# Optimization experiments

Measured on AMD Instinct MI355X. Metric: run time of the kernel, lower is better.

The kernel has to match this reference:

```python
import jax, jax.numpy as jnp
import numpy as np

D_MODEL = 1024
D_HIDDEN = 4096
NUM_EXPERTS = 8
K_ACTIVE = 2


def setup_inputs() -> dict:
    key = jax.random.key(0)
    ks = jax.random.split(key, 8)
    x = jax.random.normal(ks[0], (1, 2048, D_MODEL), dtype=jnp.float32)
    gate_w = jax.random.normal(ks[1], (D_MODEL, NUM_EXPERTS), dtype=jnp.float32) * 0.02
    gate_b = jnp.zeros((NUM_EXPERTS,), dtype=jnp.float32)
    w1 = jax.random.normal(ks[2], (NUM_EXPERTS, D_MODEL, D_HIDDEN), dtype=jnp.float32) * 0.02
    b1 = jnp.zeros((NUM_EXPERTS, D_HIDDEN), dtype=jnp.float32)
    w2 = jax.random.normal(ks[3], (NUM_EXPERTS, D_HIDDEN, D_MODEL), dtype=jnp.float32) * 0.02
    b2 = jnp.zeros((NUM_EXPERTS, D_MODEL), dtype=jnp.float32)
    return {"x": x, "gate_w": gate_w, "gate_b": gate_b,
            "w1": w1, "b1": b1, "w2": w2, "b2": b2}


def reference(x, gate_w, gate_b, w1, b1, w2, b2):
    B, S, D = x.shape
    xf = x.reshape(-1, D)                                    # [T, D]
    logits = xf @ gate_w + gate_b                            # [T, E]
    top_w, top_idx = jax.lax.top_k(logits, K_ACTIVE)         # [T, K]
    top_w = jax.nn.softmax(top_w, axis=-1)                   # softmax over selected experts
    # combine-weight per expert: sum over k slots of one-hot(idx) * weight -> [T, E]
    gates = jnp.sum(jax.nn.one_hot(top_idx, NUM_EXPERTS, dtype=xf.dtype) * top_w[..., None], axis=1)
    # expert FFN applied per expert (dropout is identity in eval): gelu is exact (erf), matching torch nn.GELU default
    h = jax.nn.gelu(jnp.einsum('td,edh->teh', xf, w1) + b1[None], approximate=False)  # [T, E, H]
    y = jnp.einsum('teh,ehd->ted', h, w2) + b2[None]         # [T, E, D]
    out = jnp.einsum('ted,te->td', y, gates)                 # weighted combine of selected experts
    return out.reshape(B, S, D)
```

## Files before the change

### kernel.cpp

```cpp
#include <hip/hip_runtime.h>
#include <stdint.h>

typedef unsigned short u16;
typedef __attribute__((ext_vector_type(8))) short s16x8;
typedef __attribute__((ext_vector_type(8))) u16  u16x8;
typedef __attribute__((ext_vector_type(4))) u16  u16x4;
typedef __attribute__((ext_vector_type(4))) float f32x4;

#define T_TOKENS 2048
#define DM 1024
#define DH 4096
#define NE 8
#define BK 64
#define PAD2 256
#define MAXS2 (T_TOKENS*2 + NE*PAD2)
#define RB1 (MAXS2/256)
#define RB2 (MAXS2/128)
#define BM 128
#define BN 128
#define MAXSLOTS (T_TOKENS*2 + NE*BM)
#define ROWBLK (MAXSLOTS/BM)

__device__ __forceinline__ u16 f2bf(float f) {
    union { float ff; uint32_t u; } v; v.ff = f;
    uint32_t r = v.u + 0x7fffu + ((v.u >> 16) & 1u);
    return (u16)(r >> 16);
}

#define GLOAD_LDS16(gsrc, ldst) \
    __builtin_amdgcn_global_load_lds((const __attribute__((address_space(1))) uint32_t*)(gsrc), \
                                     (__attribute__((address_space(3))) uint32_t*)(ldst), 16, 0, 0)

#define WAIT_VM8() asm volatile("s_waitcnt vmcnt(8)" ::: "memory")
#define WAIT_VM0() asm volatile("s_waitcnt vmcnt(0)" ::: "memory")

__global__ void k_convert(const float* __restrict__ x, u16* __restrict__ xbf,
                          int* __restrict__ ctrl) {
    int i = blockIdx.x * blockDim.x + threadIdx.x;
    const f32x4* xv = (const f32x4*)x;
    f32x4 a = xv[2*i], b = xv[2*i+1];
    u16x8 o;
    o[0]=f2bf(a[0]); o[1]=f2bf(a[1]); o[2]=f2bf(a[2]); o[3]=f2bf(a[3]);
    o[4]=f2bf(b[0]); o[5]=f2bf(b[1]); o[6]=f2bf(b[2]); o[7]=f2bf(b[3]);
    ((u16x8*)xbf)[i] = o;
    if (blockIdx.x == 0 && threadIdx.x < 32) ctrl[threadIdx.x] = 0;
}

__global__ void __launch_bounds__(256) k_transpose(const float* __restrict__ src,
                                                   u16* __restrict__ dst,
                                                   int K, int N, int nw0, int NW) {
    __shared__ float tile[64][65];
    const int e = blockIdx.z;
    const int n0 = nw0 + blockIdx.x * 64, k0 = blockIdx.y * 64;
    const float* s = src + (size_t)e * K * N;
    u16* d = dst + (size_t)e * K * NW;
    const int tx = threadIdx.x & 15, ty = threadIdx.x >> 4;
    #pragma unroll
    for (int j = 0; j < 4; ++j) {
        int r = ty * 4 + j;
        f32x4 v = *(const f32x4*)(s + (size_t)(k0 + r) * N + n0 + tx * 4);
        tile[r][tx*4+0] = v[0]; tile[r][tx*4+1] = v[1];
        tile[r][tx*4+2] = v[2]; tile[r][tx*4+3] = v[3];
    }
    __syncthreads();
    #pragma unroll
    for (int j = 0; j < 4; ++j) {
        int n = ty * 4 + j;
        u16x4 w;
        #pragma unroll
        for (int c = 0; c < 4; ++c) w[c] = f2bf(tile[tx*4+c][n]);
        *(u16x4*)(d + (size_t)(n0 - nw0 + n) * K + k0 + tx * 4) = w;
    }
}

__global__ void __launch_bounds__(64) k_gate(const float* __restrict__ x,
                                             const float* __restrict__ gw,
                                             const float* __restrict__ gb,
                                             int* __restrict__ cnt,
                                             int* __restrict__ tt_idx,
                                             float* __restrict__ tt_w) {
    const int t = blockIdx.x;
    const int lane = threadIdx.x;
    float acc[NE] = {0.f,0.f,0.f,0.f,0.f,0.f,0.f,0.f};
    const float* xr = x + (size_t)t * DM;
    #pragma unroll
    for (int c = 0; c < DM/64; ++c) {
        float xv = xr[lane + 64*c];
        const float* g = gw + (size_t)(lane + 64*c) * NE;
        #pragma unroll
        for (int e = 0; e < NE; ++e) acc[e] += xv * g[e];
    }
    #pragma unroll
    for (int e = 0; e < NE; ++e) {
        #pragma unroll
        for (int off = 32; off >= 1; off >>= 1)
            acc[e] += __shfl_xor(acc[e], off, 64);
    }
    if (lane == 0) {
        float l[NE];
        #pragma unroll
        for (int e = 0; e < NE; ++e) l[e] = acc[e] + gb[e];
        int i0 = 0;
        #pragma unroll
        for (int e = 1; e < NE; ++e) if (l[e] > l[i0]) i0 = e;
        int i1 = (i0 == 0) ? 1 : 0;
        #pragma unroll
        for (int e = 0; e < NE; ++e) if (e != i0 && l[e] > l[i1]) i1 = e;
        float m  = l[i0];
        float w0 = expf(l[i0] - m), w1 = expf(l[i1] - m);
        float s = w0 + w1; w0 /= s; w1 /= s;
        tt_idx[t*2] = i0; tt_idx[t*2+1] = i1;
        tt_w[t*2] = w0;  tt_w[t*2+1] = w1;
        atomicAdd(&cnt[i0], 1); atomicAdd(&cnt[i1], 1);
    }
}

__global__ void k_offsets(const int* __restrict__ cnt, int* __restrict__ fill,
                          int* __restrict__ off, int pad) {
    if (threadIdx.x == 0 && blockIdx.x == 0) {
        int a = 0;
        for (int e = 0; e < NE; ++e) {
            off[e] = a;
            a += (cnt[e] + pad - 1) / pad * pad;
            fill[e] = 0;
        }
        off[NE] = a;
    }
}

__global__ void k_scatter(const int* __restrict__ tt_idx, const float* __restrict__ tt_w,
                          const int* __restrict__ off, int* __restrict__ fill,
                          int* __restrict__ slot_token, float* __restrict__ slot_gate) {
    int t = blockIdx.x * blockDim.x + threadIdx.x;
    if (t >= T_TOKENS) return;
    #pragma unroll
    for (int k = 0; k < 2; ++k) {
        int e = tt_idx[t*2+k];
        int pos = off[e] + atomicAdd(&fill[e], 1);
        slot_token[pos] = t;
        slot_gate[pos]  = tt_w[t*2+k];
    }
}

__device__ __forceinline__ void mma64(const u16* As, const u16* Bs, int lane,
                                      int wr, int wc, f32x4 acc[4][4]) {
    #pragma unroll
    for (int ko = 0; ko < 2; ++ko) {
        s16x8 af[4], bfr[4];
        #pragma unroll
        for (int m = 0; m < 4; ++m) {
            int row = wr*64 + m*16 + (lane & 15);
            int sl = (ko*4 + (lane >> 4)) ^ (row & 7);
            af[m] = *(const s16x8*)&As[row*BK + sl*8];
        }
        #pragma unroll
        for (int n = 0; n < 4; ++n) {
            int col = wc*64 + n*16 + (lane & 15);
            int sl = (ko*4 + (lane >> 4)) ^ (col & 7);
            bfr[n] = *(const s16x8*)&Bs[col*BK + sl*8];
        }
        #pragma unroll
        for (int m = 0; m < 4; ++m)
            #pragma unroll
            for (int n = 0; n < 4; ++n)
                acc[m][n] = __builtin_amdgcn_mfma_f32_16x16x32_bf16(af[m], bfr[n], acc[m][n], 0, 0, 0);
    }
}

__global__ void __launch_bounds__(512, 4) k_ffn1_b16(
    const u16* __restrict__ xbf, const u16* __restrict__ wt,
    const float* __restrict__ b1, const int* __restrict__ slot_token,
    const int* __restrict__ off, u16* __restrict__ h, int cb0, int NW)
{
    __shared__ u16 As[256*BK];
    __shared__ u16 Bs[128*BK];
    const int rb = blockIdx.y, cbl = blockIdx.x;
    const int total = off[NE];
    const int r0 = rb * 256;
    if (r0 >= total) return;
    int e = 0;
    while (e < NE-1 && off[e+1] <= r0) e++;
    const u16* Bsrc = wt + (size_t)e * DM * NW;
    const float* be = b1 + (size_t)e * DH;
    const int colbase = (cb0 + cbl) * 128;

    const int tid = threadIdx.x;
    const int lane = tid & 63, wid = tid >> 6;
    const int wr = wid >> 1, wc = wid & 1;

    const u16* gA[4]; const u16* gB[2];
    #pragma unroll
    for (int i = 0; i < 4; ++i) {
        int row = wid*32 + i*8 + (lane >> 3);
        int g = (lane & 7) ^ (row & 7);
        int tok = slot_token[r0 + row];
        gA[i] = xbf + (size_t)tok * DM + g*8;
    }
    #pragma unroll
    for (int i = 0; i < 2; ++i) {
        int n = wid*16 + i*8 + (lane >> 3);
        int g = (lane & 7) ^ (n & 7);
        gB[i] = Bsrc + (size_t)(cbl*128 + n) * DM + g*8;
    }

    f32x4 acc[4][4];
    #pragma unroll
    for (int m = 0; m < 4; ++m)
        #pragma unroll
        for (int n = 0; n < 4; ++n) acc[m][n] = (f32x4){0.f,0.f,0.f,0.f};

    const int NT = DM / BK;
    #pragma unroll 1
    for (int kt = 0; kt < NT; ++kt) {
        #pragma unroll
        for (int i = 0; i < 4; ++i)
            GLOAD_LDS16(gA[i] + kt*BK, &As[(wid*32 + i*8)*BK]);
        #pragma unroll
        for (int i = 0; i < 2; ++i)
            GLOAD_LDS16(gB[i] + kt*BK, &Bs[(wid*16 + i*8)*BK]);
        __syncthreads();
        mma64(As, Bs, lane, wr, wc, acc);
        __syncthreads();
    }

    #pragma unroll
    for (int n = 0; n < 4; ++n) {
        int col = colbase + wc*64 + n*16 + (lane & 15);
        float bb = be[col];
        #pragma unroll
        for (int m = 0; m < 4; ++m) {
            int rbase = r0 + wr*64 + m*16 + (lane >> 4)*4;
            #pragma unroll
            for (int i = 0; i < 4; ++i) {
                float v = acc[m][n][i] + bb;
                float gv = 0.5f * v * (1.0f + erff(v * 0.70710678118654752f));
                h[(size_t)(rbase + i)*DH + col] = f2bf(gv);
            }
        }
    }
}

__global__ void __launch_bounds__(256) k_ffn2_b16(
    const u16* __restrict__ h, const u16* __restrict__ w2t,
    const float* __restrict__ b2, const int* __restrict__ slot_token,
    const float* __restrict__ slot_gate, const int* __restrict__ off,
    float* __restrict__ out)
{
    __shared__ u16 As[2][BM*BK];
    __shared__ u16 Bs[2][BN*BK];
    const int rb = blockIdx.y, cb = blockIdx.x;
    const int total = off[NE];
    const int r0 = rb * BM;
    if (r0 >= total) return;
    int e = 0;
    while (e < NE-1 && off[e+1] <= r0) e++;
    const u16* Bsrc = w2t + (size_t)e * DH * DM;
    const float* be = b2 + (size_t)e * DM;

    const int tid = threadIdx.x;
    const int lane = tid & 63, wid = tid >> 6;
    const int wr = wid >> 1, wc = wid & 1;

    const u16* gA[4]; const u16* gB[4];
    #pragma unroll
    for (int i = 0; i < 4; ++i) {
        int row = wid*32 + i*8 + (lane >> 3);
        int g = (lane & 7) ^ (row & 7);
        gA[i] = h + (size_t)(r0 + row) * DH + g*8;
        gB[i] = Bsrc + (size_t)(cb*BN + row) * DH + g*8;
    }

    f32x4 acc[4][4];
    #pragma unroll
    for (int m = 0; m < 4; ++m)
        #pragma unroll
        for (int n = 0; n < 4; ++n) acc[m][n] = (f32x4){0.f,0.f,0.f,0.f};

    #define STG2(buf, kt) do {                                                \
        _Pragma("unroll")                                                     \
        for (int i = 0; i < 4; ++i) {                                         \
            GLOAD_LDS16(gA[i] + (kt)*BK, &As[buf][(wid*32 + i*8)*BK]);        \
            GLOAD_LDS16(gB[i] + (kt)*BK, &Bs[buf][(wid*32 + i*8)*BK]);        \
        }                                                                     \
    } while (0)

    const int NT = DH / BK;
    STG2(0, 0);
    STG2(1, 1);
    #pragma unroll 1
    for (int kt = 0; kt < NT; ++kt) {
        if (kt + 1 < NT) WAIT_VM8(); else WAIT_VM0();
        __builtin_amdgcn_s_barrier();
        __builtin_amdgcn_s_setprio(1);
        mma64(As[kt & 1], Bs[kt & 1], lane, wr, wc, acc);
        __builtin_amdgcn_s_setprio(0);
        __builtin_amdgcn_s_barrier();
        if (kt + 2 < NT) STG2(kt & 1, kt + 2);
    }
    #undef STG2

    float bb[4];
    #pragma unroll
    for (int n = 0; n < 4; ++n) bb[n] = be[cb*BN + wc*64 + n*16 + (lane & 15)];
    #pragma unroll
    for (int m = 0; m < 4; ++m) {
        #pragma unroll
        for (int i = 0; i < 4; ++i) {
            int s = r0 + wr*64 + m*16 + (lane >> 4)*4 + i;
            int tok = slot_token[s];
            float g = slot_gate[s];
            if (g != 0.0f) {
                float* orow = out + (size_t)tok * DM + cb*BN + wc*64;
                #pragma unroll
                for (int n = 0; n < 4; ++n)
                    atomicAdd(orow + n*16 + (lane & 15), g * (acc[m][n][i] + bb[n]));
            }
        }
    }
}


__global__ void __launch_bounds__(256) k_ffn1_f32(
    const u16* __restrict__ xbf, const float* __restrict__ w1,
    const float* __restrict__ b1, const int* __restrict__ slot_token,
    const int* __restrict__ off, u16* __restrict__ h)
{
    __shared__ u16 As[BM*BK];
    __shared__ u16 Bs[BN*BK];
    const int rb = blockIdx.y, cb = blockIdx.x;
    const int total = off[NE];
    const int r0 = rb * BM;
    if (r0 >= total) return;
    int e = 0;
    while (e < NE-1 && off[e+1] <= r0) e++;
    const float* Bsrc = w1 + (size_t)e * DM * DH;
    const float* be   = b1 + (size_t)e * DH;

    const int tid = threadIdx.x;
    const int lane = tid & 63, wid = tid >> 6;
    const int wr = wid >> 1, wc = wid & 1;

    const u16* gA[4];
    #pragma unroll
    for (int i = 0; i < 4; ++i) {
        int row = wid*32 + i*8 + (lane >> 3);
        int g = (lane & 7) ^ (row & 7);
        int tok = slot_token[r0 + row];
        gA[i] = xbf + (size_t)tok * DM + g*8;
    }
    const int tc = tid & 31, tr = tid >> 5;
    const float* gB = Bsrc + (size_t)(tr*8) * DH + cb*BN + tc*4;

    f32x4 acc[4][4];
    #pragma unroll
    for (int m = 0; m < 4; ++m)
        #pragma unroll
        for (int n = 0; n < 4; ++n) acc[m][n] = (f32x4){0.f,0.f,0.f,0.f};

    for (int kt = 0; kt < DM/BK; ++kt) {
        #pragma unroll
        for (int i = 0; i < 4; ++i)
            GLOAD_LDS16(gA[i] + kt*BK, &As[(wid*32 + i*8)*BK]);
        f32x4 bv[8];
        #pragma unroll
        for (int j = 0; j < 8; ++j)
            bv[j] = *(const f32x4*)(gB + (size_t)(kt*BK + j) * DH);
        #pragma unroll
        for (int c = 0; c < 4; ++c) {
            int n = tc*4 + c;
            int sl = tr ^ (n & 7);
            s16x8 pk;
            #pragma unroll
            for (int j = 0; j < 8; ++j) pk[j] = (short)f2bf(bv[j][c]);
            *(s16x8*)&Bs[n*BK + sl*8] = pk;
        }
        __syncthreads();
        mma64(As, Bs, lane, wr, wc, acc);
        __syncthreads();
    }
    #pragma unroll
    for (int n = 0; n < 4; ++n) {
        int col = cb*BN + wc*64 + n*16 + (lane & 15);
        float bb = be[col];
        #pragma unroll
        for (int m = 0; m < 4; ++m) {
            int rbase = r0 + wr*64 + m*16 + (lane >> 4)*4;
            #pragma unroll
            for (int i = 0; i < 4; ++i) {
                float v = acc[m][n][i] + bb;
                float gv = 0.5f * v * (1.0f + erff(v * 0.70710678118654752f));
                h[(size_t)(rbase + i)*DH + col] = f2bf(gv);
            }
        }
    }
}

__global__ void __launch_bounds__(256) k_ffn2_f32(
    const u16* __restrict__ h, const float* __restrict__ w2,
    const float* __restrict__ b2, const int* __restrict__ slot_token,
    const float* __restrict__ slot_gate, const int* __restrict__ off,
    float* __restrict__ out)
{
    __shared__ u16 As[BM*BK];
    __shared__ u16 Bs[BN*BK];
    const int rb = blockIdx.y, cb = blockIdx.x;
    const int total = off[NE];
    const int r0 = rb * BM;
    if (r0 >= total) return;
    int e = 0;
    while (e < NE-1 && off[e+1] <= r0) e++;
    const float* Bsrc = w2 + (size_t)e * DH * DM;
    const float* be   = b2 + (size_t)e * DM;

    const int tid = threadIdx.x;
    const int lane = tid & 63, wid = tid >> 6;
    const int wr = wid >> 1, wc = wid & 1;

    const u16* gA[4];
    #pragma unroll
    for (int i = 0; i < 4; ++i) {
        int row = wid*32 + i*8 + (lane >> 3);
        int g = (lane & 7) ^ (row & 7);
        gA[i] = h + (size_t)(r0 + row) * DH + g*8;
    }
    const int tc = tid & 31, tr = tid >> 5;
    const float* gB = Bsrc + (size_t)(tr*8) * DM + cb*BN + tc*4;

    f32x4 acc[4][4];
    #pragma unroll
    for (int m = 0; m < 4; ++m)
        #pragma unroll
        for (int n = 0; n < 4; ++n) acc[m][n] = (f32x4){0.f,0.f,0.f,0.f};

    for (int kt = 0; kt < DH/BK; ++kt) {
        #pragma unroll
        for (int i = 0; i < 4; ++i)
            GLOAD_LDS16(gA[i] + kt*BK, &As[(wid*32 + i*8)*BK]);
        f32x4 bv[8];
        #pragma unroll
        for (int j = 0; j < 8; ++j)
            bv[j] = *(const f32x4*)(gB + (size_t)(kt*BK + j) * DM);
        #pragma unroll
        for (int c = 0; c < 4; ++c) {
            int n = tc*4 + c;
            int sl = tr ^ (n & 7);
            s16x8 pk;
            #pragma unroll
            for (int j = 0; j < 8; ++j) pk[j] = (short)f2bf(bv[j][c]);
            *(s16x8*)&Bs[n*BK + sl*8] = pk;
        }
        __syncthreads();
        mma64(As, Bs, lane, wr, wc, acc);
        __syncthreads();
    }
    float bb[4];
    #pragma unroll
    for (int n = 0; n < 4; ++n) bb[n] = be[cb*BN + wc*64 + n*16 + (lane & 15)];
    #pragma unroll
    for (int m = 0; m < 4; ++m) {
        #pragma unroll
        for (int i = 0; i < 4; ++i) {
            int s = r0 + wr*64 + m*16 + (lane >> 4)*4 + i;
            int tok = slot_token[s];
            float g = slot_gate[s];
            if (g != 0.0f) {
                float* orow = out + (size_t)tok * DM + cb*BN + wc*64;
                #pragma unroll
                for (int n = 0; n < 4; ++n)
                    atomicAdd(orow + n*16 + (lane & 15), g * (acc[m][n][i] + bb[n]));
            }
        }
    }
}

extern "C" void kernel_launch(void* const* d_in, const int* in_sizes, int n_in,
                              void* d_out, int out_size, void* d_ws, size_t ws_size,
                              hipStream_t stream)
{
    (void)in_sizes; (void)n_in; (void)out_size;
    const float* x  = (const float*)d_in[0];
    const float* gw = (const float*)d_in[1];
    const float* gb = (const float*)d_in[2];
    const float* w1 = (const float*)d_in[3];
    const float* b1 = (const float*)d_in[4];
    const float* w2 = (const float*)d_in[5];
    const float* b2 = (const float*)d_in[6];
    float* out = (float*)d_out;
    char* ws = (char*)d_ws;

    const size_t OFF_XBF = 0;
    const size_t OFF_H   = 4194304;
    const size_t OFF_ST  = OFF_H + (size_t)MAXS2 * DH * 2;
    const size_t OFF_SG  = OFF_ST + MAXS2 * 4;
    const size_t OFF_TI  = OFF_SG + MAXS2 * 4;
    const size_t OFF_TW  = OFF_TI + T_TOKENS * 2 * 4;
    const size_t OFF_CT  = OFF_TW + T_TOKENS * 2 * 4;
    const size_t OFF_WT  = (OFF_CT + 128 + 255) & ~(size_t)255;
    const size_t NEED_FULL = OFF_WT + (size_t)NE * DM * DH * 2;
    const size_t NEED_HALF = OFF_WT + (size_t)NE * DM * (DH/2) * 2;

    if (ws_size >= NEED_HALF) {
        u16*   xbf        = (u16*)(ws + OFF_XBF);
        u16*   h          = (u16*)(ws + OFF_H);
        int*   slot_token = (int*)(ws + OFF_ST);
        float* slot_gate  = (float*)(ws + OFF_SG);
        int*   tt_idx     = (int*)(ws + OFF_TI);
        float* tt_w       = (float*)(ws + OFF_TW);
        int*   ctrl       = (int*)(ws + OFF_CT);
        u16*   wt         = (u16*)(ws + OFF_WT);
        int* cnt = ctrl; int* fill = ctrl + 8; int* offs = ctrl + 16;
        const int full = (ws_size >= NEED_FULL);

        hipMemsetAsync(slot_token, 0, 2 * MAXS2 * 4, stream);
        hipMemsetAsync(out, 0, (size_t)T_TOKENS * DM * sizeof(float), stream);

        k_convert<<<(T_TOKENS*DM/8 + 255)/256, 256, 0, stream>>>(x, xbf, ctrl);
        k_gate<<<T_TOKENS, 64, 0, stream>>>(x, gw, gb, cnt, tt_idx, tt_w);
        k_offsets<<<1, 64, 0, stream>>>(cnt, fill, offs, PAD2);
        k_scatter<<<(T_TOKENS + 255)/256, 256, 0, stream>>>(tt_idx, tt_w, offs, fill,
                                                            slot_token, slot_gate);
        if (full) {
            k_transpose<<<dim3(DH/64, DM/64, NE), 256, 0, stream>>>(w1, wt, DM, DH, 0, DH);
            k_ffn1_b16<<<dim3(DH/128, RB1), 512, 0, stream>>>(xbf, wt, b1, slot_token, offs, h, 0, DH);
        } else {
            k_transpose<<<dim3(DH/128, DM/64, NE), 256, 0, stream>>>(w1, wt, DM, DH, 0, DH/2);
            k_ffn1_b16<<<dim3(DH/256, RB1), 512, 0, stream>>>(xbf, wt, b1, slot_token, offs, h, 0, DH/2);
            k_transpose<<<dim3(DH/128, DM/64, NE), 256, 0, stream>>>(w1, wt, DM, DH, DH/2, DH/2);
            k_ffn1_b16<<<dim3(DH/256, RB1), 512, 0, stream>>>(xbf, wt, b1, slot_token, offs, h, DH/256, DH/2);
        }
        k_transpose<<<dim3(DM/64, DH/64, NE), 256, 0, stream>>>(w2, wt, DH, DM, 0, DM);
        k_ffn2_b16<<<dim3(DM/BN, RB2), 256, 0, stream>>>(h, wt, b2, slot_token, slot_gate, offs, out);
    } else {
        u16*   xbf        = (u16*)(ws);
        u16*   h          = (u16*)(ws + 4194304);
        int*   slot_token = (int*)(ws + 46137344);
        float* slot_gate  = (float*)(ws + 46157824);
        int*   tt_idx     = (int*)(ws + 46178304);
        float* tt_w       = (float*)(ws + 46194688);
        int*   ctrl       = (int*)(ws + 46211072);
        int* cnt = ctrl; int* fill = ctrl + 8; int* offs = ctrl + 16;

        hipMemsetAsync(slot_token, 0, 2 * MAXSLOTS * 4, stream);
        hipMemsetAsync(out, 0, (size_t)T_TOKENS * DM * sizeof(float), stream);

        k_convert<<<(T_TOKENS*DM/8 + 255)/256, 256, 0, stream>>>(x, xbf, ctrl);
        k_gate<<<T_TOKENS, 64, 0, stream>>>(x, gw, gb, cnt, tt_idx, tt_w);
        k_offsets<<<1, 64, 0, stream>>>(cnt, fill, offs, BM);
        k_scatter<<<(T_TOKENS + 255)/256, 256, 0, stream>>>(tt_idx, tt_w, offs, fill,
                                                            slot_token, slot_gate);
        k_ffn1_f32<<<dim3(DH/BN, ROWBLK), 256, 0, stream>>>(xbf, w1, b1, slot_token, offs, h);
        k_ffn2_f32<<<dim3(DM/BN, ROWBLK), 256, 0, stream>>>(h, w2, b2, slot_token, slot_gate, offs, out);
    }
}
```

Measured before the change: 307.0 us.

## Triple-buffer LDS pipelines in both FFN GEMMs and widen ffn2 to 512 threads

Measured after the change: 385.9 us. 1.26x slower.

```diff
diff --git a/kernel.cpp b/kernel.cpp
--- a/kernel.cpp
+++ b/kernel.cpp
@@ -31,7 +31,8 @@
     __builtin_amdgcn_global_load_lds((const __attribute__((address_space(1))) uint32_t*)(gsrc), \
                                      (__attribute__((address_space(3))) uint32_t*)(ldst), 16, 0, 0)
 
-#define WAIT_VM8() asm volatile("s_waitcnt vmcnt(8)" ::: "memory")
+#define WAIT_VM6() asm volatile("s_waitcnt vmcnt(6)" ::: "memory")
+#define WAIT_VM4() asm volatile("s_waitcnt vmcnt(4)" ::: "memory")
 #define WAIT_VM0() asm volatile("s_waitcnt vmcnt(0)" ::: "memory")
 
 __global__ void k_convert(const float* __restrict__ x, u16* __restrict__ xbf,
@@ -167,13 +168,39 @@
     }
 }
 
-__global__ void __launch_bounds__(512, 4) k_ffn1_b16(
+__device__ __forceinline__ void mma64_n2(const u16* As, const u16* Bs, int lane,
+                                         int wr, int wc, f32x4 acc[4][2]) {
+    #pragma unroll
+    for (int ko = 0; ko < 2; ++ko) {
+        s16x8 af[4], bfr[2];
+        #pragma unroll
+        for (int m = 0; m < 4; ++m) {
+            int row = wr*64 + m*16 + (lane & 15);
+            int sl = (ko*4 + (lane >> 4)) ^ (row & 7);
+            af[m] = *(const s16x8*)&As[row*BK + sl*8];
+        }
+        #pragma unroll
+        for (int n = 0; n < 2; ++n) {
+            int col = wc*32 + n*16 + (lane & 15);
+            int sl = (ko*4 + (lane >> 4)) ^ (col & 7);
+            bfr[n] = *(const s16x8*)&Bs[col*BK + sl*8];
+        }
+        #pragma unroll
+        for (int m = 0; m < 4; ++m)
+            #pragma unroll
+            for (int n = 0; n < 2; ++n)
+                acc[m][n] = __builtin_amdgcn_mfma_f32_16x16x32_bf16(af[m], bfr[n], acc[m][n], 0, 0, 0);
+    }
+}
+
+
+__global__ void __launch_bounds__(512, 2) k_ffn1_b16(
     const u16* __restrict__ xbf, const u16* __restrict__ wt,
     const float* __restrict__ b1, const int* __restrict__ slot_token,
     const int* __restrict__ off, u16* __restrict__ h, int cb0, int NW)
 {
-    __shared__ u16 As[256*BK];
-    __shared__ u16 Bs[128*BK];
+    __shared__ u16 As[3][256*BK];
+    __shared__ u16 Bs[3][128*BK];
     const int rb = blockIdx.y, cbl = blockIdx.x;
     const int total = off[NE];
     const int r0 = rb * 256;
@@ -209,19 +236,31 @@
         #pragma unroll
         for (int n = 0; n < 4; ++n) acc[m][n] = (f32x4){0.f,0.f,0.f,0.f};
 
+    #define STG1(buf, kt) do {                                                \
+        _Pragma("unroll")                                                     \
+        for (int i = 0; i < 4; ++i)                                           \
+            GLOAD_LDS16(gA[i] + (kt)*BK, &As[buf][(wid*32 + i*8)*BK]);        \
+        _Pragma("unroll")                                                     \
+        for (int i = 0; i < 2; ++i)                                           \
+            GLOAD_LDS16(gB[i] + (kt)*BK, &Bs[buf][(wid*16 + i*8)*BK]);        \
+    } while (0)
+
     const int NT = DM / BK;
+    STG1(0, 0);
+    STG1(1, 1);
+    int cur = 0, stg = 2;
     #pragma unroll 1
     for (int kt = 0; kt < NT; ++kt) {
-        #pragma unroll
-        for (int i = 0; i < 4; ++i)
-            GLOAD_LDS16(gA[i] + kt*BK, &As[(wid*32 + i*8)*BK]);
-        #pragma unroll
-        for (int i = 0; i < 2; ++i)
-            GLOAD_LDS16(gB[i] + kt*BK, &Bs[(wid*16 + i*8)*BK]);
-        __syncthreads();
-        mma64(As, Bs, lane, wr, wc, acc);
-        __syncthreads();
-    }
+        if (kt + 1 < NT) WAIT_VM6(); else WAIT_VM0();
+        __builtin_amdgcn_s_barrier();
+        if (kt + 2 < NT) STG1(stg, kt + 2);
+        __builtin_amdgcn_s_setprio(1);
+        mma64(As[cur], Bs[cur], lane, wr, wc, acc);
+        __builtin_amdgcn_s_setprio(0);
+        cur = (cur == 2) ? 0 : cur + 1;
+        stg = (stg == 2) ? 0 : stg + 1;
+    }
+    #undef STG1
 
     #pragma unroll
     for (int n = 0; n < 4; ++n) {
@@ -240,14 +279,14 @@
     }
 }
 
-__global__ void __launch_bounds__(256) k_ffn2_b16(
+__global__ void __launch_bounds__(512, 2) k_ffn2_b16(
     const u16* __restrict__ h, const u16* __restrict__ w2t,
     const float* __restrict__ b2, const int* __restrict__ slot_token,
     const float* __restrict__ slot_gate, const int* __restrict__ off,
     float* __restrict__ out)
 {
-    __shared__ u16 As[2][BM*BK];
-    __shared__ u16 Bs[2][BN*BK];
+    __shared__ u16 As[3][BM*BK];
+    __shared__ u16 Bs[3][BN*BK];
     const int rb = blockIdx.y, cb = blockIdx.x;
     const int total = off[NE];
     const int r0 = rb * BM;
@@ -259,49 +298,51 @@
 
     const int tid = threadIdx.x;
     const int lane = tid & 63, wid = tid >> 6;
-    const int wr = wid >> 1, wc = wid & 1;
-
-    const u16* gA[4]; const u16* gB[4];
-    #pragma unroll
-    for (int i = 0; i < 4; ++i) {
-        int row = wid*32 + i*8 + (lane >> 3);
+    const int wr = wid >> 2, wc = wid & 3;
+
+    const u16* gA[2]; const u16* gB[2];
+    #pragma unroll
+    for (int i = 0; i < 2; ++i) {
+        int row = wid*16 + i*8 + (lane >> 3);
         int g = (lane & 7) ^ (row & 7);
         gA[i] = h + (size_t)(r0 + row) * DH + g*8;
         gB[i] = Bsrc + (size_t)(cb*BN + row) * DH + g*8;
     }
 
-    f32x4 acc[4][4];
+    f32x4 acc[4][2];
     #pragma unroll
     for (int m = 0; m < 4; ++m)
         #pragma unroll
-        for (int n = 0; n < 4; ++n) acc[m][n] = (f32x4){0.f,0.f,0.f,0.f};
+        for (int n = 0; n < 2; ++n) acc[m][n] = (f32x4){0.f,0.f,0.f,0.f};
 
     #define STG2(buf, kt) do {                                                \
         _Pragma("unroll")                                                     \
-        for (int i = 0; i < 4; ++i) {                                         \
-            GLOAD_LDS16(gA[i] + (kt)*BK, &As[buf][(wid*32 + i*8)*BK]);        \
-            GLOAD_LDS16(gB[i] + (kt)*BK, &Bs[buf][(wid*32 + i*8)*BK]);        \
+        for (int i = 0; i < 2; ++i) {                                         \
+            GLOAD_LDS16(gA[i] + (kt)*BK, &As[buf][(wid*16 + i*8)*BK]);        \
+            GLOAD_LDS16(gB[i] + (kt)*BK, &Bs[buf][(wid*16 + i*8)*BK]);        \
         }                                                                     \
     } while (0)
 
     const int NT = DH / BK;
     STG2(0, 0);
     STG2(1, 1);
+    int cur = 0, stg = 2;
     #pragma unroll 1
     for (int kt = 0; kt < NT; ++kt) {
-        if (kt + 1 < NT) WAIT_VM8(); else WAIT_VM0();
+        if (kt + 1 < NT) WAIT_VM4(); else WAIT_VM0();
         __builtin_amdgcn_s_barrier();
+        if (kt + 2 < NT) STG2(stg, kt + 2);
         __builtin_amdgcn_s_setprio(1);
-        mma64(As[kt & 1], Bs[kt & 1], lane, wr, wc, acc);
+        mma64_n2(As[cur], Bs[cur], lane, wr, wc, acc);
         __builtin_amdgcn_s_setprio(0);
-        __builtin_amdgcn_s_barrier();
-        if (kt + 2 < NT) STG2(kt & 1, kt + 2);
+        cur = (cur == 2) ? 0 : cur + 1;
+        stg = (stg == 2) ? 0 : stg + 1;
     }
     #undef STG2
 
-    float bb[4];
-    #pragma unroll
-    for (int n = 0; n < 4; ++n) bb[n] = be[cb*BN + wc*64 + n*16 + (lane & 15)];
+    float bb[2];
+    #pragma unroll
+    for (int n = 0; n < 2; ++n) bb[n] = be[cb*BN + wc*32 + n*16 + (lane & 15)];
     #pragma unroll
     for (int m = 0; m < 4; ++m) {
         #pragma unroll
@@ -310,9 +351,9 @@
             int tok = slot_token[s];
             float g = slot_gate[s];
             if (g != 0.0f) {
-                float* orow = out + (size_t)tok * DM + cb*BN + wc*64;
+                float* orow = out + (size_t)tok * DM + cb*BN + wc*32;
                 #pragma unroll
-                for (int n = 0; n < 4; ++n)
+                for (int n = 0; n < 2; ++n)
                     atomicAdd(orow + n*16 + (lane & 15), g * (acc[m][n][i] + bb[n]));
             }
         }
@@ -529,7 +570,7 @@
             k_ffn1_b16<<<dim3(DH/256, RB1), 512, 0, stream>>>(xbf, wt, b1, slot_token, offs, h, DH/256, DH/2);
         }
         k_transpose<<<dim3(DM/64, DH/64, NE), 256, 0, stream>>>(w2, wt, DH, DM, 0, DM);
-        k_ffn2_b16<<<dim3(DM/BN, RB2), 256, 0, stream>>>(h, wt, b2, slot_token, slot_gate, offs, out);
+        k_ffn2_b16<<<dim3(DM/BN, RB2), 512, 0, stream>>>(h, wt, b2, slot_token, slot_gate, offs, out);
     } else {
         u16*   xbf        = (u16*)(ws);
         u16*   h          = (u16*)(ws + 4194304);
```

## Use 128-row double-buffered FFN1 tiles, split-K FFN2, and bias pre-init

Applied to the files above, without the earlier changes.

New measurement: 335.8 us. 1.09x slower.

```diff
diff --git a/kernel.cpp b/kernel.cpp
--- a/kernel.cpp
+++ b/kernel.cpp
@@ -12,10 +12,6 @@
 #define DH 4096
 #define NE 8
 #define BK 64
-#define PAD2 256
-#define MAXS2 (T_TOKENS*2 + NE*PAD2)
-#define RB1 (MAXS2/256)
-#define RB2 (MAXS2/128)
 #define BM 128
 #define BN 128
 #define MAXSLOTS (T_TOKENS*2 + NE*BM)
@@ -142,6 +138,22 @@
     }
 }
 
+__global__ void __launch_bounds__(256) k_binit(const float* __restrict__ b2,
+                                               const int* __restrict__ tt_idx,
+                                               const float* __restrict__ tt_w,
+                                               float* __restrict__ out) {
+    const int t = blockIdx.x;
+    const int d = threadIdx.x * 4;
+    const int e0 = tt_idx[t*2], e1 = tt_idx[t*2+1];
+    const float g0 = tt_w[t*2], g1 = tt_w[t*2+1];
+    f32x4 b0 = *(const f32x4*)(b2 + (size_t)e0 * DM + d);
+    f32x4 b1 = *(const f32x4*)(b2 + (size_t)e1 * DM + d);
+    f32x4 o;
+    #pragma unroll
+    for (int c = 0; c < 4; ++c) o[c] = g0 * b0[c] + g1 * b1[c];
+    *(f32x4*)(out + (size_t)t * DM + d) = o;
+}
+
 __device__ __forceinline__ void mma64(const u16* As, const u16* Bs, int lane,
                                       int wr, int wc, f32x4 acc[4][4]) {
     #pragma unroll
@@ -167,40 +179,36 @@
     }
 }
 
-__global__ void __launch_bounds__(512, 4) k_ffn1_b16(
+
+__global__ void __launch_bounds__(256) k_ffn1_b16(
     const u16* __restrict__ xbf, const u16* __restrict__ wt,
     const float* __restrict__ b1, const int* __restrict__ slot_token,
     const int* __restrict__ off, u16* __restrict__ h, int cb0, int NW)
 {
-    __shared__ u16 As[256*BK];
-    __shared__ u16 Bs[128*BK];
+    __shared__ u16 As[2][BM*BK];
+    __shared__ u16 Bs[2][BN*BK];
     const int rb = blockIdx.y, cbl = blockIdx.x;
     const int total = off[NE];
-    const int r0 = rb * 256;
+    const int r0 = rb * BM;
     if (r0 >= total) return;
     int e = 0;
     while (e < NE-1 && off[e+1] <= r0) e++;
     const u16* Bsrc = wt + (size_t)e * DM * NW;
     const float* be = b1 + (size_t)e * DH;
-    const int colbase = (cb0 + cbl) * 128;
+    const int colbase = (cb0 + cbl) * BN;
 
     const int tid = threadIdx.x;
     const int lane = tid & 63, wid = tid >> 6;
     const int wr = wid >> 1, wc = wid & 1;
 
-    const u16* gA[4]; const u16* gB[2];
+    const u16* gA[4]; const u16* gB[4];
     #pragma unroll
     for (int i = 0; i < 4; ++i) {
         int row = wid*32 + i*8 + (lane >> 3);
         int g = (lane & 7) ^ (row & 7);
         int tok = slot_token[r0 + row];
         gA[i] = xbf + (size_t)tok * DM + g*8;
-    }
-    #pragma unroll
-    for (int i = 0; i < 2; ++i) {
-        int n = wid*16 + i*8 + (lane >> 3);
-        int g = (lane & 7) ^ (n & 7);
-        gB[i] = Bsrc + (size_t)(cbl*128 + n) * DM + g*8;
+        gB[i] = Bsrc + (size_t)(cbl*BN + row) * DM + g*8;
     }
 
     f32x4 acc[4][4];
@@ -209,19 +217,28 @@
         #pragma unroll
         for (int n = 0; n < 4; ++n) acc[m][n] = (f32x4){0.f,0.f,0.f,0.f};
 
+    #define STG1(buf, kt) do {                                                \
+        _Pragma("unroll")                                                     \
+        for (int i = 0; i < 4; ++i) {                                         \
+            GLOAD_LDS16(gA[i] + (kt)*BK, &As[buf][(wid*32 + i*8)*BK]);        \
+            GLOAD_LDS16(gB[i] + (kt)*BK, &Bs[buf][(wid*32 + i*8)*BK]);        \
+        }                                                                     \
+    } while (0)
+
     const int NT = DM / BK;
+    STG1(0, 0);
+    STG1(1, 1);
     #pragma unroll 1
     for (int kt = 0; kt < NT; ++kt) {
-        #pragma unroll
-        for (int i = 0; i < 4; ++i)
-            GLOAD_LDS16(gA[i] + kt*BK, &As[(wid*32 + i*8)*BK]);
-        #pragma unroll
-        for (int i = 0; i < 2; ++i)
-            GLOAD_LDS16(gB[i] + kt*BK, &Bs[(wid*16 + i*8)*BK]);
-        __syncthreads();
-        mma64(As, Bs, lane, wr, wc, acc);
-        __syncthreads();
-    }
+        if (kt + 1 < NT) WAIT_VM8(); else WAIT_VM0();
+        __builtin_amdgcn_s_barrier();
+        __builtin_amdgcn_s_setprio(1);
+        mma64(As[kt & 1], Bs[kt & 1], lane, wr, wc, acc);
+        __builtin_amdgcn_s_setprio(0);
+        __builtin_amdgcn_s_barrier();
+        if (kt + 2 < NT) STG1(kt & 1, kt + 2);
+    }
+    #undef STG1
 
     #pragma unroll
     for (int n = 0; n < 4; ++n) {
@@ -242,20 +259,19 @@
 
 __global__ void __launch_bounds__(256) k_ffn2_b16(
     const u16* __restrict__ h, const u16* __restrict__ w2t,
-    const float* __restrict__ b2, const int* __restrict__ slot_token,
-    const float* __restrict__ slot_gate, const int* __restrict__ off,
-    float* __restrict__ out)
+    const int* __restrict__ slot_token, const float* __restrict__ slot_gate,
+    const int* __restrict__ off, float* __restrict__ out)
 {
     __shared__ u16 As[2][BM*BK];
     __shared__ u16 Bs[2][BN*BK];
-    const int rb = blockIdx.y, cb = blockIdx.x;
+    const int rb = blockIdx.y, cb = blockIdx.x, kz = blockIdx.z;
     const int total = off[NE];
     const int r0 = rb * BM;
     if (r0 >= total) return;
     int e = 0;
     while (e < NE-1 && off[e+1] <= r0) e++;
     const u16* Bsrc = w2t + (size_t)e * DH * DM;
-    const float* be = b2 + (size_t)e * DM;
+    const int k0 = kz * (DH/2);
 
     const int tid = threadIdx.x;
     const int lane = tid & 63, wid = tid >> 6;
@@ -266,8 +282,8 @@
     for (int i = 0; i < 4; ++i) {
         int row = wid*32 + i*8 + (lane >> 3);
         int g = (lane & 7) ^ (row & 7);
-        gA[i] = h + (size_t)(r0 + row) * DH + g*8;
-        gB[i] = Bsrc + (size_t)(cb*BN + row) * DH + g*8;
+        gA[i] = h + (size_t)(r0 + row) * DH + k0 + g*8;
+        gB[i] = Bsrc + (size_t)(cb*BN + row) * DH + k0 + g*8;
     }
 
     f32x4 acc[4][4];
@@ -284,7 +300,7 @@
         }                                                                     \
     } while (0)
 
-    const int NT = DH / BK;
+    const int NT = DH / BK / 2;
     STG2(0, 0);
     STG2(1, 1);
     #pragma unroll 1
@@ -299,9 +315,6 @@
     }
     #undef STG2
 
-    float bb[4];
-    #pragma unroll
-    for (int n = 0; n < 4; ++n) bb[n] = be[cb*BN + wc*64 + n*16 + (lane & 15)];
     #pragma unroll
     for (int m = 0; m < 4; ++m) {
         #pragma unroll
@@ -313,7 +326,7 @@
                 float* orow = out + (size_t)tok * DM + cb*BN + wc*64;
                 #pragma unroll
                 for (int n = 0; n < 4; ++n)
-                    atomicAdd(orow + n*16 + (lane & 15), g * (acc[m][n][i] + bb[n]));
+                    atomicAdd(orow + n*16 + (lane & 15), g * acc[m][n][i]);
             }
         }
     }
@@ -490,9 +503,9 @@
 
     const size_t OFF_XBF = 0;
     const size_t OFF_H   = 4194304;
-    const size_t OFF_ST  = OFF_H + (size_t)MAXS2 * DH * 2;
-    const size_t OFF_SG  = OFF_ST + MAXS2 * 4;
-    const size_t OFF_TI  = OFF_SG + MAXS2 * 4;
+    const size_t OFF_ST  = OFF_H + (size_t)MAXSLOTS * DH * 2;
+    const size_t OFF_SG  = OFF_ST + MAXSLOTS * 4;
+    const size_t OFF_TI  = OFF_SG + MAXSLOTS * 4;
     const size_t OFF_TW  = OFF_TI + T_TOKENS * 2 * 4;
     const size_t OFF_CT  = OFF_TW + T_TOKENS * 2 * 4;
     const size_t OFF_WT  = (OFF_CT + 128 + 255) & ~(size_t)255;
@@ -511,33 +524,34 @@
         int* cnt = ctrl; int* fill = ctrl + 8; int* offs = ctrl + 16;
         const int full = (ws_size >= NEED_FULL);
 
-        hipMemsetAsync(slot_token, 0, 2 * MAXS2 * 4, stream);
-        hipMemsetAsync(out, 0, (size_t)T_TOKENS * DM * sizeof(float), stream);
+        hipMemsetAsync(slot_token, 0, 2 * MAXSLOTS * 4, stream);
 
         k_convert<<<(T_TOKENS*DM/8 + 255)/256, 256, 0, stream>>>(x, xbf, ctrl);
         k_gate<<<T_TOKENS, 64, 0, stream>>>(x, gw, gb, cnt, tt_idx, tt_w);
-        k_offsets<<<1, 64, 0, stream>>>(cnt, fill, offs, PAD2);
+        k_offsets<<<1, 64, 0, stream>>>(cnt, fill, offs, BM);
         k_scatter<<<(T_TOKENS + 255)/256, 256, 0, stream>>>(tt_idx, tt_w, offs, fill,
                                                             slot_token, slot_gate);
+        k_binit<<<T_TOKENS, 256, 0, stream>>>(b2, tt_idx, tt_w, out);
+
         if (full) {
             k_transpose<<<dim3(DH/64, DM/64, NE), 256, 0, stream>>>(w1, wt, DM, DH, 0, DH);
-            k_ffn1_b16<<<dim3(DH/128, RB1), 512, 0, stream>>>(xbf, wt, b1, slot_token, offs, h, 0, DH);
+            k_ffn1_b16<<<dim3(DH/BN, ROWBLK), 256, 0, stream>>>(xbf, wt, b1, slot_token, offs, h, 0, DH);
         } else {
             k_transpose<<<dim3(DH/128, DM/64, NE), 256, 0, stream>>>(w1, wt, DM, DH, 0, DH/2);
-            k_ffn1_b16<<<dim3(DH/256, RB1), 512, 0, stream>>>(xbf, wt, b1, slot_token, offs, h, 0, DH/2);
+            k_ffn1_b16<<<dim3(DH/256, ROWBLK), 256, 0, stream>>>(xbf, wt, b1, slot_token, offs, h, 0, DH/2);
             k_transpose<<<dim3(DH/128, DM/64, NE), 256, 0, stream>>>(w1, wt, DM, DH, DH/2, DH/2);
-            k_ffn1_b16<<<dim3(DH/256, RB1), 512, 0, stream>>>(xbf, wt, b1, slot_token, offs, h, DH/256, DH/2);
+            k_ffn1_b16<<<dim3(DH/256, ROWBLK), 256, 0, stream>>>(xbf, wt, b1, slot_token, offs, h, DH/256, DH/2);
         }
         k_transpose<<<dim3(DM/64, DH/64, NE), 256, 0, stream>>>(w2, wt, DH, DM, 0, DM);
-        k_ffn2_b16<<<dim3(DM/BN, RB2), 256, 0, stream>>>(h, wt, b2, slot_token, slot_gate, offs, out);
+        k_ffn2_b16<<<dim3(DM/BN, ROWBLK, 2), 256, 0, stream>>>(h, wt, slot_token, slot_gate, offs, out);
     } else {
         u16*   xbf        = (u16*)(ws);
-        u16*   h          = (u16*)(ws + 4194304);
-        int*   slot_token = (int*)(ws + 46137344);
-        float* slot_gate  = (float*)(ws + 46157824);
-        int*   tt_idx     = (int*)(ws + 46178304);
-        float* tt_w       = (float*)(ws + 46194688);
-        int*   ctrl       = (int*)(ws + 46211072);
+        u16*   h          = (u16*)(ws + OFF_H);
+        int*   slot_token = (int*)(ws + OFF_ST);
+        float* slot_gate  = (float*)(ws + OFF_SG);
+        int*   tt_idx     = (int*)(ws + OFF_TI);
+        float* tt_w       = (float*)(ws + OFF_TW);
+        int*   ctrl       = (int*)(ws + OFF_CT);
         int* cnt = ctrl; int* fill = ctrl + 8; int* offs = ctrl + 16;
 
         hipMemsetAsync(slot_token, 0, 2 * MAXSLOTS * 4, stream);
```
